# Performance work log

Hardware: AMD Instinct MI355X
Metric: run time of the kernel (lower is better)

## Reference

```python
import jax, jax.numpy as jnp
import numpy as np

NUM_BINS = 3
TAIL_BOUND = 1.0


def conv3x3(x, w, b):
    # x: [B,C,H,W], w: [O,I,3,3]
    y = jax.lax.conv_general_dilated(x, w, (1, 1), 'SAME',
                                     dimension_numbers=('NCHW', 'OIHW', 'NCHW'))
    return y + b[None, :, None, None]


def unconstrained_linear_spline(inputs, unnormalized_pdf, tail_bound=TAIL_BOUND):
    # inputs: [B,C,H,W]; unnormalized_pdf: [B,C,H,W,num_bins]
    num_bins = unnormalized_pdf.shape[-1]
    left = bottom = -tail_bound
    right = top = tail_bound
    inside = (inputs >= left) & (inputs <= right)

    x = (inputs - left) / (right - left)  # scale to [0,1]
    pdf = jax.nn.softmax(unnormalized_pdf, axis=-1)
    cdf = jnp.cumsum(pdf, axis=-1)
    cdf = cdf.at[..., -1].set(1.0)
    cdf = jnp.pad(cdf, [(0, 0)] * (cdf.ndim - 1) + [(1, 0)])  # [..., num_bins+1]

    pos = jnp.clip(x, 0.0, 1.0) * num_bins  # clip keeps bin idx valid for outside elems
    bin_idx = jnp.clip(jnp.floor(pos).astype(jnp.int32), 0, num_bins - 1)
    alpha = pos - bin_idx.astype(pos.dtype)

    input_pdfs = jnp.take_along_axis(pdf, bin_idx[..., None], axis=-1)[..., 0]
    out = jnp.take_along_axis(cdf, bin_idx[..., None], axis=-1)[..., 0] + alpha * input_pdfs
    out = jnp.clip(out, 0.0, 1.0)
    lad = jnp.log(input_pdfs) + jnp.log(jnp.asarray(num_bins, pos.dtype))

    out = out * (top - bottom) + bottom
    lad = lad - jnp.log(jnp.asarray(top - bottom, pos.dtype)) + jnp.log(jnp.asarray(right - left, pos.dtype))

    out = jnp.where(inside, out, inputs)       # identity tails
    lad = jnp.where(inside, lad, 0.0)
    return out, lad


def setup_inputs() -> dict:
    key = jax.random.key(0)
    ks = jax.random.split(key, 4)
    B, C, H, W = 32, 64, 64, 64
    hidden = 128
    c_half = C // 2
    c_out = c_half * NUM_BINS
    x = jax.random.normal(ks[0], (B, C, H, W), dtype=jnp.float32)
    objective = jnp.zeros((B,), dtype=jnp.float32)
    W1 = jax.random.normal(ks[1], (hidden, c_half, 3, 3), dtype=jnp.float32) * 0.05
    b1 = jnp.zeros((hidden,), dtype=jnp.float32)
    W2 = jax.random.normal(ks[2], (c_out, hidden, 3, 3), dtype=jnp.float32) * 0.05
    b2 = jnp.zeros((c_out,), dtype=jnp.float32)
    return {'x': x, 'objective': objective, 'W1': W1, 'b1': b1, 'W2': W2, 'b2': b2}


def reference(x, objective, W1, b1, W2, b2):
    identity_split, transform_split = jnp.split(x, 2, axis=1)
    h = jax.nn.relu(conv3x3(identity_split, W1, b1))
    transform_params = conv3x3(h, W2, b2)  # [B, C/2*num_bins, H, W]
    b, c, hh, ww = transform_split.shape
    transform_params = transform_params.reshape(b, c, NUM_BINS, hh, ww).transpose(0, 1, 3, 4, 2)
    transformed, logabsdet = unconstrained_linear_spline(transform_split, transform_params)
    output = jnp.concatenate([identity_split, transformed], axis=1)
    objective_out = objective + jnp.sum(logabsdet.reshape(b, -1), axis=1)
    return output, objective_out
```

## Files before the change

### kernel.cpp

```cpp
#include <hip/hip_runtime.h>

typedef __attribute__((ext_vector_type(8))) __bf16 bf16x8;
typedef __attribute__((ext_vector_type(4))) float f32x4;

__device__ __forceinline__ unsigned short f2bf(float f) {
    unsigned int u = __builtin_bit_cast(unsigned int, f);
    u = (u + 0x7FFFu + ((u >> 16) & 1u)) >> 16;
    return (unsigned short)u;
}

__global__ void __launch_bounds__(256) prep_w(const float* __restrict__ W1,
                                              const float* __restrict__ W2,
                                              unsigned short* __restrict__ Wt1,
                                              unsigned short* __restrict__ Wt2) {
    int tid = blockIdx.x * 256 + threadIdx.x;
    if (tid < 36864) {
        int tt = tid % 9, rem = tid / 9;
        int i = rem & 31, o = rem >> 5;
        Wt1[(tt * 128 + o) * 32 + i] = f2bf(W1[tid]);
    }
    if (tid < 110592) {
        int tt = tid % 9, rem = tid / 9;
        int i = rem & 127, o = rem >> 7;
        int kc = i >> 6, ii = i & 63;
        int khalf = ii >> 5, kgrp = (ii >> 3) & 3, j = ii & 7;
        int o_tile = o >> 4, lrow = o & 15;
        int s = kc * 9 + tt;
        Wt2[(size_t)s * 6144 +
            (size_t)(((o_tile * 2 + khalf) * 64 + kgrp * 16 + lrow) * 8 + j)] = f2bf(W2[tid]);
    }
}

__global__ void __launch_bounds__(256) conv1_fused(const float* __restrict__ x,
                                                   const float* __restrict__ obj,
                                                   const float* __restrict__ b1,
                                                   const unsigned short* __restrict__ Wt1,
                                                   unsigned short* __restrict__ hbuf,
                                                   float* __restrict__ out) {
    const int LW = 40;
    __shared__ unsigned short sx[6 * 66 * LW];
    int wg = blockIdx.x;
    int b = wg >> 4, h0 = (wg & 15) << 2;
    int t = threadIdx.x;

#pragma unroll
    for (int j = 0; j < 8; ++j) {
        int idx = j * 256 + t;
        int c = idx >> 6, row = (idx >> 4) & 3, w4 = idx & 15;
        size_t off = (((size_t)b * 64 + c) * 64 + (h0 + row)) * 16 + w4;
        reinterpret_cast<float4*>(out)[off] =
            reinterpret_cast<const float4*>(x)[off];
    }
    if (wg == 0 && t < 32) out[8388608 + t] = obj[t];

    if (t < 48) {
        int row = t >> 3, k = t & 7;
        int col = (k & 1) ? 65 : 0, c0 = (k >> 1) * 8;
        *reinterpret_cast<uint4*>(&sx[(row * 66 + col) * LW + c0]) = uint4{0, 0, 0, 0};
    }
    {
        int w = t & 63, c4 = t >> 6;
        const float* xb = x + (size_t)b * 262144;
#pragma unroll
        for (int row = 0; row < 6; ++row) {
            int gh = h0 - 1 + row;
            if (gh >= 0 && gh < 64) {
                const float* xr = xb + (size_t)gh * 64;
#pragma unroll
                for (int co = 0; co < 8; ++co) {
                    int c = co * 4 + c4;
                    sx[(row * 66 + w + 1) * LW + c] = f2bf(xr[(size_t)c * 4096 + w]);
                }
            } else {
#pragma unroll
                for (int co = 0; co < 8; ++co) {
                    int c = co * 4 + c4;
                    sx[(row * 66 + w + 1) * LW + c] = 0;
                }
            }
        }
    }
    __syncthreads();

    int wid = t >> 6, lane = t & 63;
    int lrow = lane & 15, kgrp = lane >> 4;

    bf16x8 afr[2][9];
#pragma unroll
    for (int m2 = 0; m2 < 2; ++m2) {
        int o = (wid * 2 + m2) * 16 + lrow;
#pragma unroll
        for (int tap = 0; tap < 9; ++tap)
            afr[m2][tap] = *reinterpret_cast<const bf16x8*>(
                Wt1 + (size_t)(tap * 128 + o) * 32 + kgrp * 8);
    }

    for (int nt = 0; nt < 16; ++nt) {
        int r = nt >> 2, ww = ((nt & 3) << 4) + lrow;
        f32x4 acc0 = {0.f, 0.f, 0.f, 0.f}, acc1 = {0.f, 0.f, 0.f, 0.f};
#pragma unroll
        for (int dh = 0; dh < 3; ++dh)
#pragma unroll
            for (int dw = 0; dw < 3; ++dw) {
                int tap = dh * 3 + dw;
                bf16x8 bfr = *reinterpret_cast<const bf16x8*>(
                    &sx[((r + dh) * 66 + ww + dw) * LW + kgrp * 8]);
                acc0 = __builtin_amdgcn_mfma_f32_16x16x32_bf16(afr[0][tap], bfr, acc0, 0, 0, 0);
                acc1 = __builtin_amdgcn_mfma_f32_16x16x32_bf16(afr[1][tap], bfr, acc1, 0, 0, 0);
            }
        int hh = h0 + r;
        size_t obase = (((size_t)b * 64 + hh) * 64 + ww) * 128;
#pragma unroll
        for (int m2 = 0; m2 < 2; ++m2) {
            f32x4 a = (m2 == 0) ? acc0 : acc1;
            int o0 = (wid * 2 + m2) * 16 + kgrp * 4;
            unsigned short r4[4];
#pragma unroll
            for (int j = 0; j < 4; ++j) {
                float v = a[j] + b1[o0 + j];
                r4[j] = f2bf(fmaxf(v, 0.f));
            }
            uint2 pk;
            pk.x = (unsigned)r4[0] | ((unsigned)r4[1] << 16);
            pk.y = (unsigned)r4[2] | ((unsigned)r4[3] << 16);
            *reinterpret_cast<uint2*>(hbuf + obase + o0) = pk;
        }
    }
}

__global__ void __launch_bounds__(512) conv2_spline(const unsigned short* __restrict__ hbuf,
                                                    const float* __restrict__ b2,
                                                    const unsigned short* __restrict__ Wt2,
                                                    const float* __restrict__ x,
                                                    float* __restrict__ out) {
    const int LWA = 72;
    __shared__ __align__(16) unsigned short sa[6 * 66 * LWA];
    __shared__ __align__(16) unsigned short swd[2 * 6144];
    __shared__ float red[8];
    float* pm = reinterpret_cast<float*>(sa);

    int raw = blockIdx.x;
    int wg = (raw & 7) * 64 + (raw >> 3);
    int b = wg >> 4, h0 = (wg & 15) << 2;
    int t = threadIdx.x;
    int wid = t >> 6, lane = t & 63;
    int lrow = lane & 15, kgrp = lane >> 4;
    int mgrp = wid >> 2, ngrp = wid & 3;
    int mb = mgrp * 3;

    f32x4 acc[3][4];
#pragma unroll
    for (int i = 0; i < 3; ++i)
#pragma unroll
        for (int j = 0; j < 4; ++j) acc[i][j] = f32x4{0.f, 0.f, 0.f, 0.f};

    {
        *reinterpret_cast<uint4*>(&swd[t * 8]) =
            *reinterpret_cast<const uint4*>(Wt2 + t * 8);
        if (t < 256)
            *reinterpret_cast<uint4*>(&swd[(512 + t) * 8]) =
                *reinterpret_cast<const uint4*>(Wt2 + (512 + t) * 8);
    }

    for (int kc2 = 0; kc2 < 2; ++kc2) {
#pragma unroll
        for (int j = 0; j < 6; ++j) {
            int idx = j * 512 + t;
            int row = idx >> 9, rem = idx & 511;
            int w = rem >> 3, c0 = (rem & 7) * 8;
            int gh = h0 - 1 + row;
            uint4 v = uint4{0, 0, 0, 0};
            if (gh >= 0 && gh < 64)
                v = *reinterpret_cast<const uint4*>(
                    hbuf + (((size_t)b * 64 + gh) * 64 + w) * 128 + kc2 * 64 + c0);
            *reinterpret_cast<uint4*>(&sa[(row * 66 + (w + 1)) * LWA + c0]) = v;
        }
        if (t < 96) {
            int row = t >> 4, k = t & 15;
            int col = (k & 1) ? 65 : 0, c0 = (k >> 1) * 8;
            *reinterpret_cast<uint4*>(&sa[(row * 66 + col) * LWA + c0]) = uint4{0, 0, 0, 0};
        }
        __syncthreads();

        for (int tap = 0; tap < 9; ++tap) {
            int s = kc2 * 9 + tap;
            unsigned short* swc = swd + (s & 1) * 6144;
            unsigned short* swn = swd + ((s + 1) & 1) * 6144;
            uint4 v1, v2;
            if (s < 17) {
                const unsigned short* wsrc = Wt2 + (size_t)(s + 1) * 6144;
                v1 = *reinterpret_cast<const uint4*>(wsrc + t * 8);
                if (t < 256) v2 = *reinterpret_cast<const uint4*>(wsrc + (512 + t) * 8);
            }

            int dh = tap / 3, dw = tap % 3;
            bf16x8 wfr[3][2];
#pragma unroll
            for (int mi = 0; mi < 3; ++mi) {
                int ot = mb + mi;
                wfr[mi][0] = *reinterpret_cast<const bf16x8*>(
                    &swc[((ot * 2 + 0) * 64 + lane) * 8]);
                wfr[mi][1] = *reinterpret_cast<const bf16x8*>(
                    &swc[((ot * 2 + 1) * 64 + lane) * 8]);
            }
#pragma unroll
            for (int ni = 0; ni < 4; ++ni) {
                int nt = ngrp * 4 + ni;
                int rr = nt >> 2, wcol = (nt & 3) * 16 + lrow;
                int base = ((rr + dh) * 66 + wcol + dw) * LWA;
                bf16x8 a0 = *reinterpret_cast<const bf16x8*>(&sa[base + kgrp * 8]);
                bf16x8 a1 = *reinterpret_cast<const bf16x8*>(&sa[base + 32 + kgrp * 8]);
#pragma unroll
                for (int mi = 0; mi < 3; ++mi) {
                    acc[mi][ni] = __builtin_amdgcn_mfma_f32_16x16x32_bf16(wfr[mi][0], a0, acc[mi][ni], 0, 0, 0);
                    acc[mi][ni] = __builtin_amdgcn_mfma_f32_16x16x32_bf16(wfr[mi][1], a1, acc[mi][ni], 0, 0, 0);
                }
            }
            if (s < 17) {
                *reinterpret_cast<uint4*>(&swn[t * 8]) = v1;
                if (t < 256) *reinterpret_cast<uint4*>(&swn[(512 + t) * 8]) = v2;
            }
            __syncthreads();
        }
    }

    float lad_acc = 0.f;
    for (int half = 0; half < 2; ++half) {
        __syncthreads();
        if ((ngrp >> 1) == half) {
#pragma unroll
            for (int mi = 0; mi < 3; ++mi) {
                int o0 = (mb + mi) * 16 + kgrp * 4;
                float bb0 = b2[o0], bb1 = b2[o0 + 1], bb2 = b2[o0 + 2], bb3 = b2[o0 + 3];
#pragma unroll
                for (int ni = 0; ni < 4; ++ni) {
                    int p = (ngrp & 1) * 64 + ni * 16 + lrow;
                    f32x4 v = acc[mi][ni];
                    pm[p * 101 + o0]     = v[0] + bb0;
                    pm[p * 101 + o0 + 1] = v[1] + bb1;
                    pm[p * 101 + o0 + 2] = v[2] + bb2;
                    pm[p * 101 + o0 + 3] = v[3] + bb3;
                }
            }
        }
        __syncthreads();
#pragma unroll 4
        for (int it = 0; it < 8; ++it) {
            int idx = it * 512 + t;
            int c = idx >> 7, p = idx & 127;
            int pos = half * 128 + p;
            int pb = p * 101 + 3 * c;
            float u0 = pm[pb];
            float u1 = pm[pb + 1];
            float u2 = pm[pb + 2];
            size_t gpos = (size_t)(b * 64 + 32 + c) * 4096 + (size_t)(h0 + (pos >> 6)) * 64 + (pos & 63);
            float xin = x[gpos];
            float mx = fmaxf(u0, fmaxf(u1, u2));
            float e0 = __expf(u0 - mx), e1 = __expf(u1 - mx), e2 = __expf(u2 - mx);
            float s = e0 + e1 + e2;
            float inv = 1.0f / s;
            float pos01 = fminf(fmaxf((xin + 1.f) * 0.5f, 0.f), 1.f) * 3.f;
            int bin = (int)pos01; bin = bin > 2 ? 2 : bin;
            float alpha = pos01 - (float)bin;
            float eb = (bin == 0) ? e0 : ((bin == 1) ? e1 : e2);
            float cb = (bin == 0) ? 0.f : ((bin == 1) ? e0 : (e0 + e1));
            float pk = eb * inv;
            float outv = cb * inv + alpha * pk;
            outv = fminf(fmaxf(outv, 0.f), 1.f) * 2.f - 1.f;
            float lad = __logf(pk) + 1.09861228866810969f;
            bool inside = (xin >= -1.f) && (xin <= 1.f);
            if (!inside) { outv = xin; lad = 0.f; }
            out[gpos] = outv;
            lad_acc += lad;
        }
    }
#pragma unroll
    for (int off = 32; off > 0; off >>= 1)
        lad_acc += __shfl_down(lad_acc, off, 64);
    if (lane == 0) red[wid] = lad_acc;
    __syncthreads();
    if (t == 0) {
        float s = 0.f;
#pragma unroll
        for (int i = 0; i < 8; ++i) s += red[i];
        atomicAdd(out + 8388608 + b, s);
    }
}

extern "C" void kernel_launch(void* const* d_in, const int* in_sizes, int n_in,
                              void* d_out, int out_size, void* d_ws, size_t ws_size,
                              hipStream_t stream) {
    const float* x   = (const float*)d_in[0];
    const float* obj = (const float*)d_in[1];
    const float* W1  = (const float*)d_in[2];
    const float* b1  = (const float*)d_in[3];
    const float* W2  = (const float*)d_in[4];
    const float* b2  = (const float*)d_in[5];
    float* out = (float*)d_out;
    char* ws = (char*)d_ws;

    unsigned short* hbuf = (unsigned short*)ws;
    unsigned short* Wt1  = (unsigned short*)(ws + 33554432);
    unsigned short* Wt2  = (unsigned short*)(ws + 33554432 + 73728);

    hipLaunchKernelGGL(prep_w,       dim3(432), dim3(256), 0, stream, W1, W2, Wt1, Wt2);
    hipLaunchKernelGGL(conv1_fused,  dim3(512), dim3(256), 0, stream, x, obj, b1, Wt1, hbuf, out);
    hipLaunchKernelGGL(conv2_spline, dim3(512), dim3(512), 0, stream, hbuf, b2, Wt2, x, out);
}
```

Baseline: 71.49 us.

## Load conv2 weight fragments directly from global, drop LDS double-buffer and per-tap barriers

Replaces the shared-memory double-buffered weight staging in conv2_spline with direct per-lane global loads of MFMA weight fragments, and fully unrolls the tap loop. This removes the per-tap __syncthreads and the LDS write/read traffic for weights, and frees about 24 KB of LDS, which may raise occupancy. In exchange each wave issues its own global (L2/L1-cached) weight loads with no explicit prefetch, so latency hiding now depends on the compiler scheduling loads ahead in the unrolled loop. A barrier is added before the second input-tile reload to keep LDS reuse safe.

```diff
diff --git a/kernel.cpp b/kernel.cpp
--- a/kernel.cpp
+++ b/kernel.cpp
@@ -135,7 +135,6 @@
                                                     float* __restrict__ out) {
     const int LWA = 72;
     __shared__ __align__(16) unsigned short sa[6 * 66 * LWA];
-    __shared__ __align__(16) unsigned short swd[2 * 6144];
     __shared__ float red[8];
     float* pm = reinterpret_cast<float*>(sa);
 
@@ -154,15 +153,10 @@
 #pragma unroll
         for (int j = 0; j < 4; ++j) acc[i][j] = f32x4{0.f, 0.f, 0.f, 0.f};
 
-    {
-        *reinterpret_cast<uint4*>(&swd[t * 8]) =
-            *reinterpret_cast<const uint4*>(Wt2 + t * 8);
-        if (t < 256)
-            *reinterpret_cast<uint4*>(&swd[(512 + t) * 8]) =
-                *reinterpret_cast<const uint4*>(Wt2 + (512 + t) * 8);
-    }
+    const unsigned short* wfb = Wt2 + (size_t)lane * 8;
 
     for (int kc2 = 0; kc2 < 2; ++kc2) {
+        if (kc2) __syncthreads();
 #pragma unroll
         for (int j = 0; j < 6; ++j) {
             int idx = j * 512 + t;
@@ -182,26 +176,17 @@
         }
         __syncthreads();
 
+#pragma unroll
         for (int tap = 0; tap < 9; ++tap) {
             int s = kc2 * 9 + tap;
-            unsigned short* swc = swd + (s & 1) * 6144;
-            unsigned short* swn = swd + ((s + 1) & 1) * 6144;
-            uint4 v1, v2;
-            if (s < 17) {
-                const unsigned short* wsrc = Wt2 + (size_t)(s + 1) * 6144;
-                v1 = *reinterpret_cast<const uint4*>(wsrc + t * 8);
-                if (t < 256) v2 = *reinterpret_cast<const uint4*>(wsrc + (512 + t) * 8);
-            }
-
+            const unsigned short* wsl = wfb + (size_t)s * 6144;
             int dh = tap / 3, dw = tap % 3;
             bf16x8 wfr[3][2];
 #pragma unroll
             for (int mi = 0; mi < 3; ++mi) {
                 int ot = mb + mi;
-                wfr[mi][0] = *reinterpret_cast<const bf16x8*>(
-                    &swc[((ot * 2 + 0) * 64 + lane) * 8]);
-                wfr[mi][1] = *reinterpret_cast<const bf16x8*>(
-                    &swc[((ot * 2 + 1) * 64 + lane) * 8]);
+                wfr[mi][0] = *reinterpret_cast<const bf16x8*>(wsl + (size_t)(ot * 2 + 0) * 512);
+                wfr[mi][1] = *reinterpret_cast<const bf16x8*>(wsl + (size_t)(ot * 2 + 1) * 512);
             }
 #pragma unroll
             for (int ni = 0; ni < 4; ++ni) {
@@ -216,11 +201,6 @@
                     acc[mi][ni] = __builtin_amdgcn_mfma_f32_16x16x32_bf16(wfr[mi][1], a1, acc[mi][ni], 0, 0, 0);
                 }
             }
-            if (s < 17) {
-                *reinterpret_cast<uint4*>(&swn[t * 8]) = v1;
-                if (t < 256) *reinterpret_cast<uint4*>(&swn[(512 + t) * 8]) = v2;
-            }
-            __syncthreads();
         }
     }
 
```

Result: no change. 71.02 us (-0.7%).
